# Performance work log

Hardware: AMD Instinct MI355X
Metric: run time of the kernel (lower is better)

Reference implementation:

```python
import jax, jax.numpy as jnp
import numpy as np

C = 64
DQ = C // 8  # query/key channel dim


def setup_inputs() -> dict:
    key = jax.random.key(0)
    ks = jax.random.split(key, 8)
    B, H, W = 8, 64, 64
    x = jax.random.normal(ks[0], (B, C, H, W), dtype=jnp.float32)
    # 1x1 conv weights stored as [out, in] matrices (kernel dims squeezed)
    wq = jax.random.normal(ks[1], (DQ, C), dtype=jnp.float32) * 0.05
    bq = jax.random.normal(ks[2], (DQ,), dtype=jnp.float32) * 0.05
    wk = jax.random.normal(ks[3], (DQ, C), dtype=jnp.float32) * 0.05
    bk = jax.random.normal(ks[4], (DQ,), dtype=jnp.float32) * 0.05
    wv = jax.random.normal(ks[5], (C, C), dtype=jnp.float32) * 0.05
    bv = jax.random.normal(ks[6], (C,), dtype=jnp.float32) * 0.05
    gamma = jax.random.normal(ks[7], (1,), dtype=jnp.float32)
    return {"x": x, "wq": wq, "bq": bq, "wk": wk, "bk": bk,
            "wv": wv, "bv": bv, "gamma": gamma}


def reference(x, wq, bq, wk, bk, wv, bv, gamma):
    B, Cc, H, W = x.shape
    N = H * W
    xf = x.reshape(B, Cc, N)                      # [B, C, N]
    # 1x1 convs == channel matmuls
    q = jnp.einsum('dc,bcn->bdn', wq, xf) + bq[None, :, None]   # [B, DQ, N]
    k = jnp.einsum('dc,bcn->bdn', wk, xf) + bk[None, :, None]   # [B, DQ, N]
    v = jnp.einsum('oc,bcn->bon', wv, xf) + bv[None, :, None]   # [B, C, N]
    # energy[b, m, n] = sum_d q[b, d, m] * k[b, d, n]
    energy = jnp.einsum('bdm,bdn->bmn', q, k)                   # [B, N, N]
    attention = jax.nn.softmax(energy, axis=-1)
    # out[b, c, m] = sum_n v[b, c, n] * attention[b, m, n]
    out = jnp.einsum('bcn,bmn->bcm', v, attention).reshape(B, Cc, H, W)
    return gamma[0] * out + x
```

## Files before the change

### kernel.cpp

```cpp
#include <hip/hip_runtime.h>
#include <math.h>

#define NTOK 4096
#define CCH  64
#define LOG2E 1.4426950408889634f
#define NSPLIT 2

typedef __attribute__((ext_vector_type(8)))  short bf16x8;
typedef __attribute__((ext_vector_type(4)))  float f32x4;
typedef __attribute__((ext_vector_type(16))) float f32x16;
typedef __attribute__((ext_vector_type(2)))  unsigned int uint32x2;

__device__ __forceinline__ unsigned short f2bf_rne(float f) {
    unsigned int u = __float_as_uint(f);
    u += 0x7FFFu + ((u >> 16) & 1u);
    return (unsigned short)(u >> 16);
}
__device__ __forceinline__ float bf2f(unsigned short u) {
    return __uint_as_float(((unsigned int)u) << 16);
}


__global__ __launch_bounds__(512) void proj_kernel(
    const float* __restrict__ x,
    const float* __restrict__ wq, const float* __restrict__ bq,
    const float* __restrict__ wk, const float* __restrict__ bk,
    const float* __restrict__ wv, const float* __restrict__ bv,
    unsigned short* __restrict__ qt, unsigned short* __restrict__ kt,
    unsigned short* __restrict__ vbf)
{
    __shared__ unsigned short xsb[64 * 68];
    __shared__ unsigned short wa[80 * 68];
    __shared__ unsigned short vtmp[64 * 66];
    __shared__ float bb[80];

    const int t  = threadIdx.x;
    const int b  = blockIdx.x >> 6;
    const int n0 = (blockIdx.x & 63) << 6;

    const int lane = t & 63;
    const int w    = t >> 6;
    const int l15  = lane & 15;
    const int g    = lane >> 4;
    const int nt   = w & 3;

    #pragma unroll
    for (int r = 0; r < 2; ++r) {
        const int i  = t + 512 * r;
        const int c  = i >> 4;
        const int nq = (i & 15) * 4;
        const float4 xv = *(const float4*)&x[((size_t)(b * CCH + c)) * NTOK + n0 + nq];
        xsb[(nq + 0) * 68 + c] = f2bf_rne(xv.x);
        xsb[(nq + 1) * 68 + c] = f2bf_rne(xv.y);
        xsb[(nq + 2) * 68 + c] = f2bf_rne(xv.z);
        xsb[(nq + 3) * 68 + c] = f2bf_rne(xv.w);
    }
    #pragma unroll
    for (int r = 0; r < 2; ++r) {
        const int i  = t + 512 * r;
        const int m  = i >> 4;
        const int cq = (i & 15) * 4;
        const float4 v = *(const float4*)&wv[i * 4];
        const unsigned int lo = (unsigned int)f2bf_rne(v.x) | ((unsigned int)f2bf_rne(v.y) << 16);
        const unsigned int hi = (unsigned int)f2bf_rne(v.z) | ((unsigned int)f2bf_rne(v.w) << 16);
        *(uint32x2*)&wa[m * 68 + cq] = (uint32x2){lo, hi};
    }
    if (t < 256) {
        const int half = t >> 7;
        const int j    = t & 127;
        const int m    = 64 + half * 8 + (j >> 4);
        const int cq   = (j & 15) * 4;
        const float* src = half ? wk : wq;
        const float  sc  = half ? 1.f : LOG2E;
        const float4 v = *(const float4*)&src[j * 4];
        const unsigned int lo = (unsigned int)f2bf_rne(v.x * sc) | ((unsigned int)f2bf_rne(v.y * sc) << 16);
        const unsigned int hi = (unsigned int)f2bf_rne(v.z * sc) | ((unsigned int)f2bf_rne(v.w * sc) << 16);
        *(uint32x2*)&wa[m * 68 + cq] = (uint32x2){lo, hi};
    } else if (t < 336) {
        const int j = t - 256;
        float bias;
        if (j < 64)      bias = bv[j];
        else if (j < 72) bias = bq[j - 64] * LOG2E;
        else             bias = bk[j - 72];
        bb[j] = bias;
    }
    __syncthreads();

    const int mtbase = (w < 4) ? 0 : 3;
    const int nmt    = (w < 4) ? 3 : 2;
    f32x4 acc[3];
    #pragma unroll
    for (int j = 0; j < 3; ++j) acc[j] = (f32x4){0.f, 0.f, 0.f, 0.f};
    #pragma unroll
    for (int kc = 0; kc < 2; ++kc) {
        const bf16x8 bx = *(const bf16x8*)&xsb[(nt * 16 + l15) * 68 + kc * 32 + g * 8];
        #pragma unroll
        for (int j = 0; j < 3; ++j) {
            if (j < nmt) {
                const bf16x8 aw = *(const bf16x8*)&wa[((mtbase + j) * 16 + l15) * 68 + kc * 32 + g * 8];
                acc[j] = __builtin_amdgcn_mfma_f32_16x16x32_bf16(aw, bx, acc[j], 0, 0, 0);
            }
        }
    }

    #pragma unroll
    for (int j = 0; j < 3; ++j) {
        if (j < nmt) {
            const int mt = mtbase + j;
            if (mt < 4) {
                #pragma unroll
                for (int r = 0; r < 4; ++r) {
                    const int c = mt * 16 + g * 4 + r;
                    vtmp[c * 66 + 4 * l15 + nt] = f2bf_rne(acc[j][r] + bb[c]);
                }
            } else {
                unsigned short vals[4];
                #pragma unroll
                for (int r = 0; r < 4; ++r)
                    vals[r] = f2bf_rne(acc[j][r] + bb[64 + g * 4 + r]);
                const unsigned int lo = (unsigned int)vals[0] | ((unsigned int)vals[1] << 16);
                const unsigned int hi = (unsigned int)vals[2] | ((unsigned int)vals[3] << 16);
                const int n = nt * 16 + l15;
                unsigned short* dst = ((g < 2) ? qt : kt) +
                                      ((size_t)(b * NTOK + n0 + n)) * 8 + (g & 1) * 4;
                *(uint32x2*)dst = (uint32x2){lo, hi};
            }
        }
    }
    __syncthreads();

    {
        const int c   = t >> 3;
        const int seg = t & 7;
        unsigned short* dst = vbf + ((size_t)(b * CCH + c)) * NTOK + n0 + seg * 8;
        *(bf16x8*)dst = *(const bf16x8*)&vtmp[c * 66 + seg * 8];
    }
}

__global__ __launch_bounds__(256, 6) void attn_kernel(
    const unsigned short* __restrict__ qt, const unsigned short* __restrict__ kt,
    const unsigned short* __restrict__ vbf,
    unsigned short* __restrict__ opart, float* __restrict__ lpart, int B)
{
    __shared__ unsigned short vs[64 * 88];
    __shared__ unsigned short ps[64 * 88];

    const int t    = threadIdx.x;
    const int lane = t & 63;
    const int w    = t >> 6;
    const int bid  = blockIdx.x;
    const int b    = bid % B;
    const int p    = (bid / B) % NSPLIT;
    const int m0   = (bid / (B * NSPLIT)) << 6;

    const int l15 = lane & 15;
    const int g   = lane >> 4;
    const int l31 = lane & 31;
    const int h   = lane >> 5;

    const int NIT     = 64 / NSPLIT;
    const int itStart = p * NIT;

    bf16x8 a_q = {};
    if (g == 0)
        a_q = *(const bf16x8*)&qt[((size_t)(b * NTOK + m0 + w * 16 + l15)) * 8];

    const int c0  = t >> 3, seg = t & 7;
    const int c1  = c0 + 32;
    const unsigned short* vsrc0 = vbf + ((size_t)(b * CCH + c0)) * NTOK
                                      + itStart * 64 + seg * 8;
    const unsigned short* vsrc1 = vbf + ((size_t)(b * CCH + c1)) * NTOK
                                      + itStart * 64 + seg * 8;
    unsigned short* vdst0 = &vs[c0 * 88 + seg * 8];
    unsigned short* vdst1 = &vs[c1 * 88 + seg * 8];

    const unsigned short* ksrc = kt + ((size_t)(b * NTOK + itStart * 64 + l15)) * 8;

    bf16x8 vreg0 = *(const bf16x8*)vsrc0;
    bf16x8 vreg1 = *(const bf16x8*)vsrc1;
    bf16x8 kr0 = {}, kr1 = {}, kr2 = {}, kr3 = {};
    if (g == 0) {
        kr0 = *(const bf16x8*)(ksrc);
        kr1 = *(const bf16x8*)(ksrc + 128);
        kr2 = *(const bf16x8*)(ksrc + 256);
        kr3 = *(const bf16x8*)(ksrc + 384);
    }

    f32x16 oacc;
    #pragma unroll
    for (int i = 0; i < 16; ++i) oacc[i] = 0.f;
    float rs0 = 0.f, rs1 = 0.f, rs2 = 0.f, rs3 = 0.f;

    const int crow = ((w >> 1) * 32 + l31) * 88;
    const int mrow = ((w & 1) * 32 + l31) * 88;

    for (int it = 0; it < NIT; ++it) {
        __syncthreads();

        *(bf16x8*)vdst0 = vreg0;
        *(bf16x8*)vdst1 = vreg1;

        const f32x4 z = {0.f, 0.f, 0.f, 0.f};
        f32x4 s0 = __builtin_amdgcn_mfma_f32_16x16x32_bf16(a_q, kr0, z, 0, 0, 0);
        f32x4 s1 = __builtin_amdgcn_mfma_f32_16x16x32_bf16(a_q, kr1, z, 0, 0, 0);
        f32x4 s2 = __builtin_amdgcn_mfma_f32_16x16x32_bf16(a_q, kr2, z, 0, 0, 0);
        f32x4 s3 = __builtin_amdgcn_mfma_f32_16x16x32_bf16(a_q, kr3, z, 0, 0, 0);

        if (it + 1 < NIT) {
            vsrc0 += 64;  vsrc1 += 64;  ksrc += 64 * 8;
            vreg0 = *(const bf16x8*)vsrc0;
            vreg1 = *(const bf16x8*)vsrc1;
            if (g == 0) {
                kr0 = *(const bf16x8*)(ksrc);
                kr1 = *(const bf16x8*)(ksrc + 128);
                kr2 = *(const bf16x8*)(ksrc + 256);
                kr3 = *(const bf16x8*)(ksrc + 384);
            }
        }

        #pragma unroll
        for (int r = 0; r < 4; ++r) {
            const float p0 = __builtin_amdgcn_exp2f(s0[r]);
            const float p1 = __builtin_amdgcn_exp2f(s1[r]);
            const float p2 = __builtin_amdgcn_exp2f(s2[r]);
            const float p3 = __builtin_amdgcn_exp2f(s3[r]);
            const unsigned int lo = __builtin_amdgcn_perm(
                __float_as_uint(p1), __float_as_uint(p0), 0x07060302u);
            const unsigned int hi = __builtin_amdgcn_perm(
                __float_as_uint(p3), __float_as_uint(p2), 0x07060302u);
            *(uint32x2*)&ps[(w * 16 + g * 4 + r) * 88 + 4 * l15] = (uint32x2){lo, hi};
            const float ssum = (p0 + p1) + (p2 + p3);
            if      (r == 0) rs0 += ssum;
            else if (r == 1) rs1 += ssum;
            else if (r == 2) rs2 += ssum;
            else             rs3 += ssum;
        }
        __syncthreads();

        #pragma unroll
        for (int kc = 0; kc < 4; ++kc) {
            const bf16x8 a_v = *(const bf16x8*)&vs[crow + kc * 16 + h * 8];
            const bf16x8 b_p = *(const bf16x8*)&ps[mrow + kc * 16 + h * 8];
            oacc = __builtin_amdgcn_mfma_f32_32x32x16_bf16(a_v, b_p, oacc, 0, 0, 0);
        }
    }

    #pragma unroll
    for (int xm = 1; xm <= 8; xm <<= 1) {
        rs0 += __shfl_xor(rs0, xm);
        rs1 += __shfl_xor(rs1, xm);
        rs2 += __shfl_xor(rs2, xm);
        rs3 += __shfl_xor(rs3, xm);
    }
    if (l15 == 0) {
        float* lp = lpart + (size_t)(p * B + b) * NTOK + m0 + w * 16 + g * 4;
        lp[0] = rs0; lp[1] = rs1; lp[2] = rs2; lp[3] = rs3;
    }
    {
        const int mloc = (w & 1) * 32 + l31;
        #pragma unroll
        for (int reg = 0; reg < 16; ++reg) {
            const int c = (w >> 1) * 32 + (reg & 3) + 8 * (reg >> 2) + 4 * h;
            opart[((size_t)((p * B + b) * CCH + c)) * NTOK + m0 + mloc] =
                f2bf_rne(oacc[reg]);
        }
    }
}

__global__ __launch_bounds__(256) void combine_kernel(
    const unsigned short* __restrict__ opart, const float* __restrict__ lpart,
    const float* __restrict__ x, const float* __restrict__ gamma_p,
    float* __restrict__ out, int B)
{
    const float  gm      = gamma_p[0];
    const size_t nf4     = (size_t)B * CCH * NTOK / 4;
    const size_t ostride = (size_t)B * CCH * NTOK;
    for (size_t f = (size_t)blockIdx.x * 256 + threadIdx.x; f < nf4;
         f += (size_t)gridDim.x * 256) {
        const int m4 = ((int)(f & 1023)) * 4;
        const int bc = (int)(f >> 10);
        const int bi = bc >> 6;
        const size_t obase = (size_t)bc * NTOK + m4;

        float4 osum = {0.f, 0.f, 0.f, 0.f};
        float4 lsum = {0.f, 0.f, 0.f, 0.f};
        #pragma unroll
        for (int p = 0; p < NSPLIT; ++p) {
            const ushort4 o = *(const ushort4*)&opart[obase + (size_t)p * ostride];
            const float4  l = *(const float4*)&lpart[(size_t)(p * B + bi) * NTOK + m4];
            osum.x += bf2f(o.x); osum.y += bf2f(o.y);
            osum.z += bf2f(o.z); osum.w += bf2f(o.w);
            lsum.x += l.x; lsum.y += l.y; lsum.z += l.z; lsum.w += l.w;
        }
        const float4 xv = *(const float4*)&x[obase];
        float4 r;
        r.x = osum.x * gm / lsum.x + xv.x;
        r.y = osum.y * gm / lsum.y + xv.y;
        r.z = osum.z * gm / lsum.z + xv.z;
        r.w = osum.w * gm / lsum.w + xv.w;
        *(float4*)&out[obase] = r;
    }
}

extern "C" void kernel_launch(void* const* d_in, const int* in_sizes, int n_in,
                              void* d_out, int out_size, void* d_ws, size_t ws_size,
                              hipStream_t stream) {
    const float* x     = (const float*)d_in[0];
    const float* wq    = (const float*)d_in[1];
    const float* bq    = (const float*)d_in[2];
    const float* wk    = (const float*)d_in[3];
    const float* bk    = (const float*)d_in[4];
    const float* wv    = (const float*)d_in[5];
    const float* bv    = (const float*)d_in[6];
    const float* gamma = (const float*)d_in[7];
    float* out = (float*)d_out;

    int B = in_sizes[0] / (CCH * NTOK);

    unsigned short* wsp   = (unsigned short*)d_ws;
    unsigned short* qt    = wsp;
    unsigned short* kt    = qt + (size_t)B * NTOK * 8;
    unsigned short* vbf   = kt + (size_t)B * NTOK * 8;
    unsigned short* opart = vbf + (size_t)B * CCH * NTOK;
    float*          lpart = (float*)(opart + (size_t)NSPLIT * B * CCH * NTOK);

    proj_kernel<<<B * 64, 512, 0, stream>>>(x, wq, bq, wk, bk, wv, bv, qt, kt, vbf);
    attn_kernel<<<NSPLIT * B * 64, 256, 0, stream>>>(qt, kt, vbf, opart, lpart, B);
    combine_kernel<<<1024, 256, 0, stream>>>(opart, lpart, x, gamma, out, B);
}
```

Measured before the change: 121.5 us.

## Drop key-split and fuse normalization and residual into attention epilogue

Removes the two-way split over key blocks, so each attention block processes all 64 key tiles. The softmax row sums are now normalized in shared memory and the gamma scaling plus residual add are written directly from the attention kernel. This eliminates the combine kernel launch, the bf16 partial output buffers and their round trip through memory. The cost is half as many blocks (512) in the attention grid, which lowers parallelism and occupancy on a GPU with many CUs.

```diff
diff --git a/kernel.cpp b/kernel.cpp
--- a/kernel.cpp
+++ b/kernel.cpp
@@ -4,7 +4,7 @@
 #define NTOK 4096
 #define CCH  64
 #define LOG2E 1.4426950408889634f
-#define NSPLIT 2
+#define NSPLIT 1
 
 typedef __attribute__((ext_vector_type(8)))  short bf16x8;
 typedef __attribute__((ext_vector_type(4)))  float f32x4;
@@ -140,26 +140,26 @@
 __global__ __launch_bounds__(256, 6) void attn_kernel(
     const unsigned short* __restrict__ qt, const unsigned short* __restrict__ kt,
     const unsigned short* __restrict__ vbf,
-    unsigned short* __restrict__ opart, float* __restrict__ lpart, int B)
+    const float* __restrict__ x, const float* __restrict__ gamma_p,
+    float* __restrict__ out, int B)
 {
     __shared__ unsigned short vs[64 * 88];
     __shared__ unsigned short ps[64 * 88];
+    __shared__ float ls[64];
 
     const int t    = threadIdx.x;
     const int lane = t & 63;
     const int w    = t >> 6;
     const int bid  = blockIdx.x;
     const int b    = bid % B;
-    const int p    = (bid / B) % NSPLIT;
-    const int m0   = (bid / (B * NSPLIT)) << 6;
+    const int m0   = (bid / B) << 6;
 
     const int l15 = lane & 15;
     const int g   = lane >> 4;
     const int l31 = lane & 31;
     const int h   = lane >> 5;
 
-    const int NIT     = 64 / NSPLIT;
-    const int itStart = p * NIT;
+    const int NIT = 64;
 
     bf16x8 a_q = {};
     if (g == 0)
@@ -167,14 +167,12 @@
 
     const int c0  = t >> 3, seg = t & 7;
     const int c1  = c0 + 32;
-    const unsigned short* vsrc0 = vbf + ((size_t)(b * CCH + c0)) * NTOK
-                                      + itStart * 64 + seg * 8;
-    const unsigned short* vsrc1 = vbf + ((size_t)(b * CCH + c1)) * NTOK
-                                      + itStart * 64 + seg * 8;
+    const unsigned short* vsrc0 = vbf + ((size_t)(b * CCH + c0)) * NTOK + seg * 8;
+    const unsigned short* vsrc1 = vbf + ((size_t)(b * CCH + c1)) * NTOK + seg * 8;
     unsigned short* vdst0 = &vs[c0 * 88 + seg * 8];
     unsigned short* vdst1 = &vs[c1 * 88 + seg * 8];
 
-    const unsigned short* ksrc = kt + ((size_t)(b * NTOK + itStart * 64 + l15)) * 8;
+    const unsigned short* ksrc = kt + ((size_t)(b * NTOK + l15)) * 8;
 
     bf16x8 vreg0 = *(const bf16x8*)vsrc0;
     bf16x8 vreg1 = *(const bf16x8*)vsrc1;
@@ -253,52 +251,21 @@
         rs3 += __shfl_xor(rs3, xm);
     }
     if (l15 == 0) {
-        float* lp = lpart + (size_t)(p * B + b) * NTOK + m0 + w * 16 + g * 4;
-        lp[0] = rs0; lp[1] = rs1; lp[2] = rs2; lp[3] = rs3;
-    }
+        const int mb = w * 16 + g * 4;
+        ls[mb + 0] = rs0; ls[mb + 1] = rs1; ls[mb + 2] = rs2; ls[mb + 3] = rs3;
+    }
+    __syncthreads();
+
     {
-        const int mloc = (w & 1) * 32 + l31;
+        const float gm   = gamma_p[0];
+        const int   mloc = (w & 1) * 32 + l31;
+        const float inv  = gm / ls[mloc];
         #pragma unroll
         for (int reg = 0; reg < 16; ++reg) {
             const int c = (w >> 1) * 32 + (reg & 3) + 8 * (reg >> 2) + 4 * h;
-            opart[((size_t)((p * B + b) * CCH + c)) * NTOK + m0 + mloc] =
-                f2bf_rne(oacc[reg]);
-        }
-    }
-}
-
-__global__ __launch_bounds__(256) void combine_kernel(
-    const unsigned short* __restrict__ opart, const float* __restrict__ lpart,
-    const float* __restrict__ x, const float* __restrict__ gamma_p,
-    float* __restrict__ out, int B)
-{
-    const float  gm      = gamma_p[0];
-    const size_t nf4     = (size_t)B * CCH * NTOK / 4;
-    const size_t ostride = (size_t)B * CCH * NTOK;
-    for (size_t f = (size_t)blockIdx.x * 256 + threadIdx.x; f < nf4;
-         f += (size_t)gridDim.x * 256) {
-        const int m4 = ((int)(f & 1023)) * 4;
-        const int bc = (int)(f >> 10);
-        const int bi = bc >> 6;
-        const size_t obase = (size_t)bc * NTOK + m4;
-
-        float4 osum = {0.f, 0.f, 0.f, 0.f};
-        float4 lsum = {0.f, 0.f, 0.f, 0.f};
-        #pragma unroll
-        for (int p = 0; p < NSPLIT; ++p) {
-            const ushort4 o = *(const ushort4*)&opart[obase + (size_t)p * ostride];
-            const float4  l = *(const float4*)&lpart[(size_t)(p * B + bi) * NTOK + m4];
-            osum.x += bf2f(o.x); osum.y += bf2f(o.y);
-            osum.z += bf2f(o.z); osum.w += bf2f(o.w);
-            lsum.x += l.x; lsum.y += l.y; lsum.z += l.z; lsum.w += l.w;
-        }
-        const float4 xv = *(const float4*)&x[obase];
-        float4 r;
-        r.x = osum.x * gm / lsum.x + xv.x;
-        r.y = osum.y * gm / lsum.y + xv.y;
-        r.z = osum.z * gm / lsum.z + xv.z;
-        r.w = osum.w * gm / lsum.w + xv.w;
-        *(float4*)&out[obase] = r;
+            const size_t a = ((size_t)(b * CCH + c)) * NTOK + m0 + mloc;
+            out[a] = oacc[reg] * inv + x[a];
+        }
     }
 }
 
@@ -321,10 +288,7 @@
     unsigned short* qt    = wsp;
     unsigned short* kt    = qt + (size_t)B * NTOK * 8;
     unsigned short* vbf   = kt + (size_t)B * NTOK * 8;
-    unsigned short* opart = vbf + (size_t)B * CCH * NTOK;
-    float*          lpart = (float*)(opart + (size_t)NSPLIT * B * CCH * NTOK);
 
     proj_kernel<<<B * 64, 512, 0, stream>>>(x, wq, bq, wk, bk, wv, bv, qt, kt, vbf);
-    attn_kernel<<<NSPLIT * B * 64, 256, 0, stream>>>(qt, kt, vbf, opart, lpart, B);
-    combine_kernel<<<1024, 256, 0, stream>>>(opart, lpart, x, gamma, out, B);
-}
+    attn_kernel<<<B * 64, 256, 0, stream>>>(qt, kt, vbf, x, gamma, out, B);
+}
```

After: 128.8 us. +6.0%, slower.

## Split attention block key dimension across two wave halves with LDS reduction

Applied to the files above, without the earlier changes.

The attention kernel now runs 512 threads per block: the 8 waves split each 64-key tile into two halves. Each half computes scores, exponentials and PV MFMAs for its 32 keys, and at the end partial accumulators and row sums are combined through LDS. The aim is more waves per block to hide latency, with less per-wave register and instruction work. In exchange it adds an end-of-kernel LDS reduction, extra barriers, and narrower 4-byte P stores into LDS.

```diff
diff --git a/kernel.cpp b/kernel.cpp
--- a/kernel.cpp
+++ b/kernel.cpp
@@ -137,13 +137,14 @@
     }
 }
 
-__global__ __launch_bounds__(256, 6) void attn_kernel(
+__global__ __launch_bounds__(512, 8) void attn_kernel(
     const unsigned short* __restrict__ qt, const unsigned short* __restrict__ kt,
     const unsigned short* __restrict__ vbf,
     unsigned short* __restrict__ opart, float* __restrict__ lpart, int B)
 {
-    __shared__ unsigned short vs[64 * 88];
-    __shared__ unsigned short ps[64 * 88];
+    __shared__ unsigned short lds[2 * 64 * 88];
+    unsigned short* vs = lds;
+    unsigned short* ps = lds + 64 * 88;
 
     const int t    = threadIdx.x;
     const int lane = t & 63;
@@ -157,33 +158,29 @@
     const int g   = lane >> 4;
     const int l31 = lane & 31;
     const int h   = lane >> 5;
+    const int mt  = w & 3;
+    const int hp  = w >> 2;
 
     const int NIT     = 64 / NSPLIT;
     const int itStart = p * NIT;
 
     bf16x8 a_q = {};
     if (g == 0)
-        a_q = *(const bf16x8*)&qt[((size_t)(b * NTOK + m0 + w * 16 + l15)) * 8];
-
-    const int c0  = t >> 3, seg = t & 7;
-    const int c1  = c0 + 32;
+        a_q = *(const bf16x8*)&qt[((size_t)(b * NTOK + m0 + mt * 16 + l15)) * 8];
+
+    const int c0 = t >> 3, seg = t & 7;
     const unsigned short* vsrc0 = vbf + ((size_t)(b * CCH + c0)) * NTOK
                                       + itStart * 64 + seg * 8;
-    const unsigned short* vsrc1 = vbf + ((size_t)(b * CCH + c1)) * NTOK
-                                      + itStart * 64 + seg * 8;
     unsigned short* vdst0 = &vs[c0 * 88 + seg * 8];
-    unsigned short* vdst1 = &vs[c1 * 88 + seg * 8];
-
-    const unsigned short* ksrc = kt + ((size_t)(b * NTOK + itStart * 64 + l15)) * 8;
+
+    const unsigned short* ksrc = kt +
+        ((size_t)(b * NTOK + itStart * 64 + hp * 32 + l15)) * 8;
 
     bf16x8 vreg0 = *(const bf16x8*)vsrc0;
-    bf16x8 vreg1 = *(const bf16x8*)vsrc1;
-    bf16x8 kr0 = {}, kr1 = {}, kr2 = {}, kr3 = {};
+    bf16x8 kr0 = {}, kr1 = {};
     if (g == 0) {
         kr0 = *(const bf16x8*)(ksrc);
         kr1 = *(const bf16x8*)(ksrc + 128);
-        kr2 = *(const bf16x8*)(ksrc + 256);
-        kr3 = *(const bf16x8*)(ksrc + 384);
     }
 
     f32x16 oacc;
@@ -191,30 +188,24 @@
     for (int i = 0; i < 16; ++i) oacc[i] = 0.f;
     float rs0 = 0.f, rs1 = 0.f, rs2 = 0.f, rs3 = 0.f;
 
-    const int crow = ((w >> 1) * 32 + l31) * 88;
-    const int mrow = ((w & 1) * 32 + l31) * 88;
+    const int crow = ((mt >> 1) * 32 + l31) * 88;
+    const int mrow = ((mt & 1) * 32 + l31) * 88;
 
     for (int it = 0; it < NIT; ++it) {
         __syncthreads();
 
         *(bf16x8*)vdst0 = vreg0;
-        *(bf16x8*)vdst1 = vreg1;
 
         const f32x4 z = {0.f, 0.f, 0.f, 0.f};
         f32x4 s0 = __builtin_amdgcn_mfma_f32_16x16x32_bf16(a_q, kr0, z, 0, 0, 0);
         f32x4 s1 = __builtin_amdgcn_mfma_f32_16x16x32_bf16(a_q, kr1, z, 0, 0, 0);
-        f32x4 s2 = __builtin_amdgcn_mfma_f32_16x16x32_bf16(a_q, kr2, z, 0, 0, 0);
-        f32x4 s3 = __builtin_amdgcn_mfma_f32_16x16x32_bf16(a_q, kr3, z, 0, 0, 0);
 
         if (it + 1 < NIT) {
-            vsrc0 += 64;  vsrc1 += 64;  ksrc += 64 * 8;
+            vsrc0 += 64;  ksrc += 64 * 8;
             vreg0 = *(const bf16x8*)vsrc0;
-            vreg1 = *(const bf16x8*)vsrc1;
             if (g == 0) {
                 kr0 = *(const bf16x8*)(ksrc);
                 kr1 = *(const bf16x8*)(ksrc + 128);
-                kr2 = *(const bf16x8*)(ksrc + 256);
-                kr3 = *(const bf16x8*)(ksrc + 384);
             }
         }
 
@@ -222,14 +213,10 @@
         for (int r = 0; r < 4; ++r) {
             const float p0 = __builtin_amdgcn_exp2f(s0[r]);
             const float p1 = __builtin_amdgcn_exp2f(s1[r]);
-            const float p2 = __builtin_amdgcn_exp2f(s2[r]);
-            const float p3 = __builtin_amdgcn_exp2f(s3[r]);
             const unsigned int lo = __builtin_amdgcn_perm(
                 __float_as_uint(p1), __float_as_uint(p0), 0x07060302u);
-            const unsigned int hi = __builtin_amdgcn_perm(
-                __float_as_uint(p3), __float_as_uint(p2), 0x07060302u);
-            *(uint32x2*)&ps[(w * 16 + g * 4 + r) * 88 + 4 * l15] = (uint32x2){lo, hi};
-            const float ssum = (p0 + p1) + (p2 + p3);
+            *(unsigned int*)&ps[(mt * 16 + g * 4 + r) * 88 + 4 * l15 + 2 * hp] = lo;
+            const float ssum = p0 + p1;
             if      (r == 0) rs0 += ssum;
             else if (r == 1) rs1 += ssum;
             else if (r == 2) rs2 += ssum;
@@ -237,11 +224,14 @@
         }
         __syncthreads();
 
-        #pragma unroll
-        for (int kc = 0; kc < 4; ++kc) {
-            const bf16x8 a_v = *(const bf16x8*)&vs[crow + kc * 16 + h * 8];
-            const bf16x8 b_p = *(const bf16x8*)&ps[mrow + kc * 16 + h * 8];
-            oacc = __builtin_amdgcn_mfma_f32_32x32x16_bf16(a_v, b_p, oacc, 0, 0, 0);
+        {
+            const int kc0 = hp * 2;
+            const bf16x8 av0 = *(const bf16x8*)&vs[crow + kc0 * 16 + h * 8];
+            const bf16x8 bp0 = *(const bf16x8*)&ps[mrow + kc0 * 16 + h * 8];
+            oacc = __builtin_amdgcn_mfma_f32_32x32x16_bf16(av0, bp0, oacc, 0, 0, 0);
+            const bf16x8 av1 = *(const bf16x8*)&vs[crow + (kc0 + 1) * 16 + h * 8];
+            const bf16x8 bp1 = *(const bf16x8*)&ps[mrow + (kc0 + 1) * 16 + h * 8];
+            oacc = __builtin_amdgcn_mfma_f32_32x32x16_bf16(av1, bp1, oacc, 0, 0, 0);
         }
     }
 
@@ -252,15 +242,38 @@
         rs2 += __shfl_xor(rs2, xm);
         rs3 += __shfl_xor(rs3, xm);
     }
-    if (l15 == 0) {
-        float* lp = lpart + (size_t)(p * B + b) * NTOK + m0 + w * 16 + g * 4;
-        lp[0] = rs0; lp[1] = rs1; lp[2] = rs2; lp[3] = rs3;
-    }
-    {
-        const int mloc = (w & 1) * 32 + l31;
+
+    __syncthreads();
+    float* scr = (float*)lds;
+    if (hp == 1) {
+        #pragma unroll
+        for (int r = 0; r < 16; ++r)
+            scr[mt * 1024 + r * 64 + lane] = oacc[r];
+        if (l15 == 0) {
+            const int row = mt * 16 + g * 4;
+            scr[4096 + row + 0] = rs0;
+            scr[4096 + row + 1] = rs1;
+            scr[4096 + row + 2] = rs2;
+            scr[4096 + row + 3] = rs3;
+        }
+    }
+    __syncthreads();
+    if (hp == 0) {
+        #pragma unroll
+        for (int r = 0; r < 16; ++r)
+            oacc[r] += scr[mt * 1024 + r * 64 + lane];
+        if (l15 == 0) {
+            const int row = mt * 16 + g * 4;
+            float* lp = lpart + (size_t)(p * B + b) * NTOK + m0 + row;
+            lp[0] = rs0 + scr[4096 + row + 0];
+            lp[1] = rs1 + scr[4096 + row + 1];
+            lp[2] = rs2 + scr[4096 + row + 2];
+            lp[3] = rs3 + scr[4096 + row + 3];
+        }
+        const int mloc = (mt & 1) * 32 + l31;
         #pragma unroll
         for (int reg = 0; reg < 16; ++reg) {
-            const int c = (w >> 1) * 32 + (reg & 3) + 8 * (reg >> 2) + 4 * h;
+            const int c = (mt >> 1) * 32 + (reg & 3) + 8 * (reg >> 2) + 4 * h;
             opart[((size_t)((p * B + b) * CCH + c)) * NTOK + m0 + mloc] =
                 f2bf_rne(oacc[reg]);
         }
@@ -325,6 +338,6 @@
     float*          lpart = (float*)(opart + (size_t)NSPLIT * B * CCH * NTOK);
 
     proj_kernel<<<B * 64, 512, 0, stream>>>(x, wq, bq, wk, bk, wv, bv, qt, kt, vbf);
-    attn_kernel<<<NSPLIT * B * 64, 256, 0, stream>>>(qt, kt, vbf, opart, lpart, B);
+    attn_kernel<<<NSPLIT * B * 64, 512, 0, stream>>>(qt, kt, vbf, opart, lpart, B);
     combine_kernel<<<1024, 256, 0, stream>>>(opart, lpart, x, gamma, out, B);
 }
```

Result: slower. 336.4 us (+176.8%).
